# Kernel optimization log

Hardware: AMD Instinct MI355X
Metric: run time of the kernel (lower is better)

Reference implementation:

```python
import jax, jax.numpy as jnp
import numpy as np

N, NQ, NV, NE = 4, 256, 512, 256


def setup_inputs() -> dict:
    key = jax.random.key(0)
    ks = jax.random.split(key, 6)
    scale = 1.0 / np.sqrt(NE)
    return {
        "query": jax.random.normal(ks[0], (N, NQ, NE), dtype=jnp.float32),
        "context": jax.random.normal(ks[1], (N, NV, NE), dtype=jnp.float32),
        "memory": jax.random.normal(ks[2], (N, NV, NE), dtype=jnp.float32),
        "w_logit": jax.random.normal(ks[3], (NE,), dtype=jnp.float32) * scale,
        "b_logit": jnp.zeros((), dtype=jnp.float32),
        "temp": jnp.ones((), dtype=jnp.float32),
        "w_reduce": jax.random.normal(ks[4], (NE, NE), dtype=jnp.float32) * scale,
        "b_reduce": jnp.zeros((NE,), dtype=jnp.float32),
    }


def reference(query, context, memory, w_logit, b_logit, temp, w_reduce, b_reduce):
    # Additive (Bahdanau) attention, single-head branch of the torch module.
    # qc: [N, nQ, nV, nE] -- the large broadcast-add + tanh intermediate
    qc = jnp.tanh(query[:, :, None, :] + context[:, None, :, :])
    # fc_logit: Linear(nE -> 1), squeeze last dim -> [N, nQ, nV]
    logits = jnp.einsum("nqve,e->nqv", qc, w_logit) + b_logit
    probs = jax.nn.softmax(logits / temp, axis=2)
    # bmm(probs, memory) -> [N, nQ, nE], then leaky_relu (torch default slope 0.01)
    heads = jax.nn.leaky_relu(jnp.einsum("nqv,nve->nqe", probs, memory), negative_slope=0.01)
    # fc_reduceheads: Linear(nE -> nE), torch semantics y = x @ W.T + b
    return heads @ w_reduce.T + b_reduce
```

## Files before the change

### kernel.cpp

```cpp
#include <hip/hip_runtime.h>
#include <math.h>

#define N_B   4
#define NQ_   256
#define NV_   512
#define NE_   256

#define QSCALE 2.8853900817779268f

__device__ __forceinline__ float wave_reduce_sum(float v) {
#pragma unroll
    for (int m = 32; m > 0; m >>= 1) v += __shfl_xor(v, m, 64);
    return v;
}

__global__ __launch_bounds__(256) void prep_kernel(const float* __restrict__ C,
                                                   const float* __restrict__ W,
                                                   float* __restrict__ EC,
                                                   float* __restrict__ WT) {
    __shared__ float tile[64][65];
    const int b = blockIdx.x;
    const int col = threadIdx.x & 63, row4 = threadIdx.x >> 6;
    if (b < 128) {
        const int n  = b >> 5;
        const int e0 = ((b >> 3) & 3) * 64;
        const int v0 = (b & 7) * 64;
        const float* src = C + ((size_t)n * NV_ + v0) * NE_ + e0;
#pragma unroll
        for (int r = 0; r < 16; ++r) {
            const int vl = row4 + r * 4;
            tile[vl][col] = __builtin_amdgcn_exp2f(src[(size_t)vl * NE_ + col] * QSCALE);
        }
        __syncthreads();
        float* dst = EC + ((size_t)n * NE_ + e0) * NV_ + v0;
#pragma unroll
        for (int r = 0; r < 16; ++r) {
            const int el = row4 + r * 4;
            dst[(size_t)el * NV_ + col] = tile[col][el];
        }
    } else {
        const int bb = b - 128;
        const int r0 = (bb >> 2) * 64, c0 = (bb & 3) * 64;
        const float* src = W + (size_t)r0 * NE_ + c0;
#pragma unroll
        for (int r = 0; r < 16; ++r) {
            const int rl = row4 + r * 4;
            tile[rl][col] = src[(size_t)rl * NE_ + col];
        }
        __syncthreads();
        float* dst = WT + (size_t)c0 * NE_ + r0;
#pragma unroll
        for (int r = 0; r < 16; ++r) {
            const int cl = row4 + r * 4;
            dst[(size_t)cl * NE_ + col] = tile[col][cl];
        }
    }
}

#define QTA 4
__global__ __launch_bounds__(256, 8) void logits_kernel(
    const float* __restrict__ Q,
    const float* __restrict__ EC,
    const float* __restrict__ WL,
    float* __restrict__ S)
{
    const int n  = blockIdx.z;
    const int q0 = blockIdx.y * QTA;
    const int v0 = blockIdx.x * 64;
    const int tid = threadIdx.x;
    const int wv = tid >> 6, ln = tid & 63;

    __shared__ __align__(16) float s_q[NE_][QTA];
    __shared__ float s_w[NE_];
    __shared__ float s_part[4][QTA][64];

    {
        const int e = tid;
        s_w[e] = WL[e];
#pragma unroll
        for (int j = 0; j < QTA; ++j)
            s_q[e][j] = __builtin_amdgcn_exp2f(
                Q[((size_t)n * NQ_ + q0 + j) * NE_ + e] * QSCALE);
    }
    __syncthreads();

    const float* ec = EC + (size_t)n * NE_ * NV_ + v0 + ln;
    float acc0 = 0.f, acc1 = 0.f, acc2 = 0.f, acc3 = 0.f;
    const int e0 = wv * 64;
#pragma unroll 4
    for (int e = e0; e < e0 + 64; e += 2) {
        const float c0 = ec[(size_t)e * NV_];
        const float c1 = ec[(size_t)(e + 1) * NV_];
        const float4 qa = *(const float4*)s_q[e];
        const float4 qb = *(const float4*)s_q[e + 1];
        const float w0 = s_w[e], w1 = s_w[e + 1];
        {
            const float a = fmaf(c0, qa.x, 1.0f);
            const float b = fmaf(c1, qb.x, 1.0f);
            const float num = fmaf(w1, a, w0 * b);
            acc0 = fmaf(num, __builtin_amdgcn_rcpf(a * b), acc0);
        }
        {
            const float a = fmaf(c0, qa.y, 1.0f);
            const float b = fmaf(c1, qb.y, 1.0f);
            const float num = fmaf(w1, a, w0 * b);
            acc1 = fmaf(num, __builtin_amdgcn_rcpf(a * b), acc1);
        }
        {
            const float a = fmaf(c0, qa.z, 1.0f);
            const float b = fmaf(c1, qb.z, 1.0f);
            const float num = fmaf(w1, a, w0 * b);
            acc2 = fmaf(num, __builtin_amdgcn_rcpf(a * b), acc2);
        }
        {
            const float a = fmaf(c0, qa.w, 1.0f);
            const float b = fmaf(c1, qb.w, 1.0f);
            const float num = fmaf(w1, a, w0 * b);
            acc3 = fmaf(num, __builtin_amdgcn_rcpf(a * b), acc3);
        }
    }
    s_part[wv][0][ln] = acc0;
    s_part[wv][1][ln] = acc1;
    s_part[wv][2][ln] = acc2;
    s_part[wv][3][ln] = acc3;
    __syncthreads();

    {
        const int j = tid >> 6, l = tid & 63;
        const float s = s_part[0][j][l] + s_part[1][j][l]
                      + s_part[2][j][l] + s_part[3][j][l];
        S[((size_t)n * NQ_ + q0 + j) * NV_ + v0 + l] = s;
    }
}

#define QTB 4
#define NWB 8
__global__ __launch_bounds__(512) void attn_out(
    const float* __restrict__ S,
    const float* __restrict__ M,
    const float* __restrict__ TEMP,
    const float* __restrict__ WRT,
    const float* __restrict__ BR,
    float* __restrict__ OUT)
{
    const int n  = blockIdx.y;
    const int q0 = blockIdx.x * QTB;
    const int tid = threadIdx.x;
    const int wv = tid >> 6, ln = tid & 63;

    __shared__ __align__(16) float s_prob[QTB][NV_];
    __shared__ __align__(16) float s_part[NWB][QTB][NE_];
    __shared__ __align__(16) float s_heads[QTB][NE_];

    if (wv < QTB) {
        const float scale = -2.0f / TEMP[0];
        const float* srow = S + ((size_t)n * NQ_ + q0 + wv) * NV_;
        float l[NV_ / 64];
        float mx = -1e30f;
#pragma unroll
        for (int k = 0; k < NV_ / 64; ++k) {
            l[k] = srow[ln + 64 * k] * scale;
            mx = fmaxf(mx, l[k]);
        }
#pragma unroll
        for (int m = 32; m > 0; m >>= 1) mx = fmaxf(mx, __shfl_xor(mx, m, 64));
        float sum = 0.0f;
#pragma unroll
        for (int k = 0; k < NV_ / 64; ++k) {
            l[k] = __expf(l[k] - mx);
            sum += l[k];
        }
        sum = wave_reduce_sum(sum);
        const float inv = 1.0f / sum;
#pragma unroll
        for (int k = 0; k < NV_ / 64; ++k) s_prob[wv][ln + 64 * k] = l[k] * inv;
    }
    __syncthreads();

    {
        const float4* M4 = (const float4*)(M + (size_t)n * NV_ * NE_);
        float4 h[QTB];
#pragma unroll
        for (int t = 0; t < QTB; ++t) h[t] = make_float4(0.f, 0.f, 0.f, 0.f);
        const int v0 = wv * (NV_ / NWB);
#pragma unroll 2
        for (int v = v0; v < v0 + NV_ / NWB; ++v) {
            const float4 m = M4[v * (NE_ / 4) + ln];
#pragma unroll
            for (int t = 0; t < QTB; ++t) {
                const float p = s_prob[t][v];
                h[t].x = fmaf(p, m.x, h[t].x);
                h[t].y = fmaf(p, m.y, h[t].y);
                h[t].z = fmaf(p, m.z, h[t].z);
                h[t].w = fmaf(p, m.w, h[t].w);
            }
        }
#pragma unroll
        for (int t = 0; t < QTB; ++t) ((float4*)s_part[wv][t])[ln] = h[t];
    }
    __syncthreads();

#pragma unroll
    for (int i = tid; i < QTB * NE_; i += 512) {
        const int t = i >> 8, e = i & (NE_ - 1);
        float s = 0.0f;
#pragma unroll
        for (int w = 0; w < NWB; ++w) s += s_part[w][t][e];
        s_heads[t][e] = (s > 0.0f) ? s : 0.01f * s;
    }
    __syncthreads();

    {
        const int t0 = (tid >> 8) * 2;
        const int ep = tid & 255;
        const float* w = WRT + ep;
        float a0 = 0.f, a1 = 0.f;
#pragma unroll 8
        for (int e = 0; e < NE_; ++e) {
            const float wv_ = w[(size_t)e * NE_];
            a0 = fmaf(s_heads[t0][e], wv_, a0);
            a1 = fmaf(s_heads[t0 + 1][e], wv_, a1);
        }
        const float b = BR[ep];
        OUT[((size_t)n * NQ_ + q0 + t0) * NE_ + ep]     = a0 + b;
        OUT[((size_t)n * NQ_ + q0 + t0 + 1) * NE_ + ep] = a1 + b;
    }
}

extern "C" void kernel_launch(void* const* d_in, const int* in_sizes, int n_in,
                              void* d_out, int out_size, void* d_ws, size_t ws_size,
                              hipStream_t stream) {
    const float* Q  = (const float*)d_in[0];
    const float* C  = (const float*)d_in[1];
    const float* M  = (const float*)d_in[2];
    const float* WL = (const float*)d_in[3];
    const float* T  = (const float*)d_in[5];
    const float* WR = (const float*)d_in[6];
    const float* BR = (const float*)d_in[7];
    float* OUT = (float*)d_out;

    float* EC  = (float*)d_ws;
    float* WRT = EC + (size_t)N_B * NE_ * NV_;
    float* S   = WRT + (size_t)NE_ * NE_;

    prep_kernel<<<dim3(144), 256, 0, stream>>>(C, WR, EC, WRT);

    dim3 ga(NV_ / 64, NQ_ / QTA, N_B);
    logits_kernel<<<ga, 256, 0, stream>>>(Q, EC, WL, S);

    dim3 gb(NQ_ / QTB, N_B);
    attn_out<<<gb, 512, 0, stream>>>(S, M, T, WRT, BR, OUT);
}
```

Measured before the change: 109.1 us.

## Fuse logits, softmax and output projection into one 1024-thread kernel

Merges the logits kernel and the attention-output kernel into one kernel per 4-query tile with 1024 threads. Each thread computes full logits for one v over half of e, and softmax runs directly from registers, which removes the global logits buffer and one launch. EC is repacked as interleaved e-pairs so each thread does a float2 load. In exchange the grid shrinks to 256 blocks of 1024 threads with about 70KB of shared memory, which may lower occupancy and latency hiding in the logits loop.

```diff
diff --git a/kernel.cpp b/kernel.cpp
--- a/kernel.cpp
+++ b/kernel.cpp
@@ -7,6 +7,7 @@
 #define NE_   256
 
 #define QSCALE 2.8853900817779268f
+#define QTF 4
 
 __device__ __forceinline__ float wave_reduce_sum(float v) {
 #pragma unroll
@@ -32,11 +33,12 @@
             tile[vl][col] = __builtin_amdgcn_exp2f(src[(size_t)vl * NE_ + col] * QSCALE);
         }
         __syncthreads();
-        float* dst = EC + ((size_t)n * NE_ + e0) * NV_ + v0;
-#pragma unroll
-        for (int r = 0; r < 16; ++r) {
-            const int el = row4 + r * 4;
-            dst[(size_t)el * NV_ + col] = tile[col][el];
+        float2* dst = (float2*)EC + ((size_t)n * (NE_ / 2) + (e0 >> 1)) * NV_ + v0;
+#pragma unroll
+        for (int rr = 0; rr < 8; ++rr) {
+            const int pe = rr * 4 + row4;
+            dst[(size_t)pe * NV_ + col] =
+                make_float2(tile[col][2 * pe], tile[col][2 * pe + 1]);
         }
     } else {
         const int bb = b - 128;
@@ -57,173 +59,182 @@
     }
 }
 
-#define QTA 4
-__global__ __launch_bounds__(256, 8) void logits_kernel(
+#define FMA4(h, p, m)                  \
+    h.x = fmaf(p, m.x, h.x);           \
+    h.y = fmaf(p, m.y, h.y);           \
+    h.z = fmaf(p, m.z, h.z);           \
+    h.w = fmaf(p, m.w, h.w)
+
+__global__ __launch_bounds__(1024) void fused_attn(
     const float* __restrict__ Q,
     const float* __restrict__ EC,
     const float* __restrict__ WL,
-    float* __restrict__ S)
-{
-    const int n  = blockIdx.z;
-    const int q0 = blockIdx.y * QTA;
-    const int v0 = blockIdx.x * 64;
-    const int tid = threadIdx.x;
-    const int wv = tid >> 6, ln = tid & 63;
-
-    __shared__ __align__(16) float s_q[NE_][QTA];
-    __shared__ float s_w[NE_];
-    __shared__ float s_part[4][QTA][64];
-
-    {
-        const int e = tid;
-        s_w[e] = WL[e];
-#pragma unroll
-        for (int j = 0; j < QTA; ++j)
-            s_q[e][j] = __builtin_amdgcn_exp2f(
-                Q[((size_t)n * NQ_ + q0 + j) * NE_ + e] * QSCALE);
-    }
-    __syncthreads();
-
-    const float* ec = EC + (size_t)n * NE_ * NV_ + v0 + ln;
-    float acc0 = 0.f, acc1 = 0.f, acc2 = 0.f, acc3 = 0.f;
-    const int e0 = wv * 64;
-#pragma unroll 4
-    for (int e = e0; e < e0 + 64; e += 2) {
-        const float c0 = ec[(size_t)e * NV_];
-        const float c1 = ec[(size_t)(e + 1) * NV_];
-        const float4 qa = *(const float4*)s_q[e];
-        const float4 qb = *(const float4*)s_q[e + 1];
-        const float w0 = s_w[e], w1 = s_w[e + 1];
-        {
-            const float a = fmaf(c0, qa.x, 1.0f);
-            const float b = fmaf(c1, qb.x, 1.0f);
-            const float num = fmaf(w1, a, w0 * b);
-            acc0 = fmaf(num, __builtin_amdgcn_rcpf(a * b), acc0);
-        }
-        {
-            const float a = fmaf(c0, qa.y, 1.0f);
-            const float b = fmaf(c1, qb.y, 1.0f);
-            const float num = fmaf(w1, a, w0 * b);
-            acc1 = fmaf(num, __builtin_amdgcn_rcpf(a * b), acc1);
-        }
-        {
-            const float a = fmaf(c0, qa.z, 1.0f);
-            const float b = fmaf(c1, qb.z, 1.0f);
-            const float num = fmaf(w1, a, w0 * b);
-            acc2 = fmaf(num, __builtin_amdgcn_rcpf(a * b), acc2);
-        }
-        {
-            const float a = fmaf(c0, qa.w, 1.0f);
-            const float b = fmaf(c1, qb.w, 1.0f);
-            const float num = fmaf(w1, a, w0 * b);
-            acc3 = fmaf(num, __builtin_amdgcn_rcpf(a * b), acc3);
-        }
-    }
-    s_part[wv][0][ln] = acc0;
-    s_part[wv][1][ln] = acc1;
-    s_part[wv][2][ln] = acc2;
-    s_part[wv][3][ln] = acc3;
-    __syncthreads();
-
-    {
-        const int j = tid >> 6, l = tid & 63;
-        const float s = s_part[0][j][l] + s_part[1][j][l]
-                      + s_part[2][j][l] + s_part[3][j][l];
-        S[((size_t)n * NQ_ + q0 + j) * NV_ + v0 + l] = s;
-    }
-}
-
-#define QTB 4
-#define NWB 8
-__global__ __launch_bounds__(512) void attn_out(
-    const float* __restrict__ S,
     const float* __restrict__ M,
     const float* __restrict__ TEMP,
     const float* __restrict__ WRT,
     const float* __restrict__ BR,
     float* __restrict__ OUT)
 {
-    const int n  = blockIdx.y;
-    const int q0 = blockIdx.x * QTB;
+    const int n   = blockIdx.y;
+    const int q0  = blockIdx.x * QTF;
     const int tid = threadIdx.x;
-    const int wv = tid >> 6, ln = tid & 63;
-
-    __shared__ __align__(16) float s_prob[QTB][NV_];
-    __shared__ __align__(16) float s_part[NWB][QTB][NE_];
-    __shared__ __align__(16) float s_heads[QTB][NE_];
-
-    if (wv < QTB) {
+    const int wv  = tid >> 6, ln = tid & 63;
+
+    __shared__ __align__(16) float s_q[NE_][QTF];
+    __shared__ __align__(16) float s_w[NE_];
+    __shared__ __align__(16) float s_prob[QTF][NV_];
+    __shared__ __align__(16) float s_sp[QTF][NV_];
+    __shared__ __align__(16) float s_part[16][QTF][NE_];
+    __shared__ __align__(16) float s_heads[QTF][NE_];
+    __shared__ __align__(16) float s_gp[QTF][NE_];
+    __shared__ float s_sum[QTF][8];
+
+    {
+        const int e = tid & 255;
+        const int g = tid >> 8;
+        s_q[e][g] = __builtin_amdgcn_exp2f(
+            Q[((size_t)n * NQ_ + q0 + g) * NE_ + e] * QSCALE);
+        if (g == 0) s_w[e] = WL[e];
+    }
+    __syncthreads();
+
+    const int v  = tid & 511;
+    const int eh = tid >> 9;
+    float acc0 = 0.f, acc1 = 0.f, acc2 = 0.f, acc3 = 0.f;
+    {
+        const float2* ec2 =
+            (const float2*)EC + ((size_t)n * (NE_ / 2) + eh * 64) * NV_ + v;
+#pragma unroll 4
+        for (int pe = 0; pe < 64; ++pe) {
+            const float2 c = ec2[(size_t)pe * NV_];
+            const int e = eh * 128 + 2 * pe;
+            const float4 qa = *(const float4*)s_q[e];
+            const float4 qb = *(const float4*)s_q[e + 1];
+            const float2 w  = *(const float2*)&s_w[e];
+            {
+                const float a = fmaf(c.x, qa.x, 1.0f);
+                const float b = fmaf(c.y, qb.x, 1.0f);
+                const float num = fmaf(w.y, a, w.x * b);
+                acc0 = fmaf(num, __builtin_amdgcn_rcpf(a * b), acc0);
+            }
+            {
+                const float a = fmaf(c.x, qa.y, 1.0f);
+                const float b = fmaf(c.y, qb.y, 1.0f);
+                const float num = fmaf(w.y, a, w.x * b);
+                acc1 = fmaf(num, __builtin_amdgcn_rcpf(a * b), acc1);
+            }
+            {
+                const float a = fmaf(c.x, qa.z, 1.0f);
+                const float b = fmaf(c.y, qb.z, 1.0f);
+                const float num = fmaf(w.y, a, w.x * b);
+                acc2 = fmaf(num, __builtin_amdgcn_rcpf(a * b), acc2);
+            }
+            {
+                const float a = fmaf(c.x, qa.w, 1.0f);
+                const float b = fmaf(c.y, qb.w, 1.0f);
+                const float num = fmaf(w.y, a, w.x * b);
+                acc3 = fmaf(num, __builtin_amdgcn_rcpf(a * b), acc3);
+            }
+        }
+    }
+    if (eh) {
+        s_sp[0][v] = acc0; s_sp[1][v] = acc1;
+        s_sp[2][v] = acc2; s_sp[3][v] = acc3;
+    }
+    __syncthreads();
+
+    float p0 = 0.f, p1 = 0.f, p2 = 0.f, p3 = 0.f;
+    if (!eh) {
         const float scale = -2.0f / TEMP[0];
-        const float* srow = S + ((size_t)n * NQ_ + q0 + wv) * NV_;
-        float l[NV_ / 64];
-        float mx = -1e30f;
-#pragma unroll
-        for (int k = 0; k < NV_ / 64; ++k) {
-            l[k] = srow[ln + 64 * k] * scale;
-            mx = fmaxf(mx, l[k]);
-        }
-#pragma unroll
-        for (int m = 32; m > 0; m >>= 1) mx = fmaxf(mx, __shfl_xor(mx, m, 64));
-        float sum = 0.0f;
-#pragma unroll
-        for (int k = 0; k < NV_ / 64; ++k) {
-            l[k] = __expf(l[k] - mx);
-            sum += l[k];
-        }
-        sum = wave_reduce_sum(sum);
-        const float inv = 1.0f / sum;
-#pragma unroll
-        for (int k = 0; k < NV_ / 64; ++k) s_prob[wv][ln + 64 * k] = l[k] * inv;
+        p0 = __expf((acc0 + s_sp[0][v]) * scale);
+        p1 = __expf((acc1 + s_sp[1][v]) * scale);
+        p2 = __expf((acc2 + s_sp[2][v]) * scale);
+        p3 = __expf((acc3 + s_sp[3][v]) * scale);
+        const float r0 = wave_reduce_sum(p0);
+        const float r1 = wave_reduce_sum(p1);
+        const float r2 = wave_reduce_sum(p2);
+        const float r3 = wave_reduce_sum(p3);
+        if (ln == 0) {
+            s_sum[0][wv] = r0; s_sum[1][wv] = r1;
+            s_sum[2][wv] = r2; s_sum[3][wv] = r3;
+        }
+    }
+    __syncthreads();
+    if (!eh) {
+        float t0 = 0.f, t1 = 0.f, t2 = 0.f, t3 = 0.f;
+#pragma unroll
+        for (int w = 0; w < 8; ++w) {
+            t0 += s_sum[0][w]; t1 += s_sum[1][w];
+            t2 += s_sum[2][w]; t3 += s_sum[3][w];
+        }
+        s_prob[0][v] = p0 * (1.0f / t0);
+        s_prob[1][v] = p1 * (1.0f / t1);
+        s_prob[2][v] = p2 * (1.0f / t2);
+        s_prob[3][v] = p3 * (1.0f / t3);
     }
     __syncthreads();
 
     {
         const float4* M4 = (const float4*)(M + (size_t)n * NV_ * NE_);
-        float4 h[QTB];
-#pragma unroll
-        for (int t = 0; t < QTB; ++t) h[t] = make_float4(0.f, 0.f, 0.f, 0.f);
-        const int v0 = wv * (NV_ / NWB);
+        float4 h0 = make_float4(0.f, 0.f, 0.f, 0.f);
+        float4 h1 = h0, h2 = h0, h3 = h0;
+        const int v0w = wv * 32;
 #pragma unroll 2
-        for (int v = v0; v < v0 + NV_ / NWB; ++v) {
-            const float4 m = M4[v * (NE_ / 4) + ln];
-#pragma unroll
-            for (int t = 0; t < QTB; ++t) {
-                const float p = s_prob[t][v];
-                h[t].x = fmaf(p, m.x, h[t].x);
-                h[t].y = fmaf(p, m.y, h[t].y);
-                h[t].z = fmaf(p, m.z, h[t].z);
-                h[t].w = fmaf(p, m.w, h[t].w);
-            }
-        }
-#pragma unroll
-        for (int t = 0; t < QTB; ++t) ((float4*)s_part[wv][t])[ln] = h[t];
-    }
-    __syncthreads();
-
-#pragma unroll
-    for (int i = tid; i < QTB * NE_; i += 512) {
-        const int t = i >> 8, e = i & (NE_ - 1);
-        float s = 0.0f;
-#pragma unroll
-        for (int w = 0; w < NWB; ++w) s += s_part[w][t][e];
+        for (int vb = v0w; vb < v0w + 32; vb += 4) {
+            const float4 pq0 = *(const float4*)&s_prob[0][vb];
+            const float4 pq1 = *(const float4*)&s_prob[1][vb];
+            const float4 pq2 = *(const float4*)&s_prob[2][vb];
+            const float4 pq3 = *(const float4*)&s_prob[3][vb];
+            float4 mm;
+            mm = M4[(size_t)(vb + 0) * (NE_ / 4) + ln];
+            FMA4(h0, pq0.x, mm); FMA4(h1, pq1.x, mm);
+            FMA4(h2, pq2.x, mm); FMA4(h3, pq3.x, mm);
+            mm = M4[(size_t)(vb + 1) * (NE_ / 4) + ln];
+            FMA4(h0, pq0.y, mm); FMA4(h1, pq1.y, mm);
+            FMA4(h2, pq2.y, mm); FMA4(h3, pq3.y, mm);
+            mm = M4[(size_t)(vb + 2) * (NE_ / 4) + ln];
+            FMA4(h0, pq0.z, mm); FMA4(h1, pq1.z, mm);
+            FMA4(h2, pq2.z, mm); FMA4(h3, pq3.z, mm);
+            mm = M4[(size_t)(vb + 3) * (NE_ / 4) + ln];
+            FMA4(h0, pq0.w, mm); FMA4(h1, pq1.w, mm);
+            FMA4(h2, pq2.w, mm); FMA4(h3, pq3.w, mm);
+        }
+        ((float4*)s_part[wv][0])[ln] = h0;
+        ((float4*)s_part[wv][1])[ln] = h1;
+        ((float4*)s_part[wv][2])[ln] = h2;
+        ((float4*)s_part[wv][3])[ln] = h3;
+    }
+    __syncthreads();
+
+    {
+        const int t = tid >> 8, e = tid & 255;
+        float s = 0.f;
+#pragma unroll
+        for (int w = 0; w < 16; ++w) s += s_part[w][t][e];
         s_heads[t][e] = (s > 0.0f) ? s : 0.01f * s;
     }
     __syncthreads();
 
     {
-        const int t0 = (tid >> 8) * 2;
-        const int ep = tid & 255;
-        const float* w = WRT + ep;
+        const int eh2 = tid >> 9;
+        const int tg  = ((tid >> 8) & 1) * 2;
+        const int ep  = tid & 255;
+        const float* wc = WRT + ep;
         float a0 = 0.f, a1 = 0.f;
+        const int e0g = eh2 * 128;
 #pragma unroll 8
-        for (int e = 0; e < NE_; ++e) {
-            const float wv_ = w[(size_t)e * NE_];
-            a0 = fmaf(s_heads[t0][e], wv_, a0);
-            a1 = fmaf(s_heads[t0 + 1][e], wv_, a1);
-        }
-        const float b = BR[ep];
-        OUT[((size_t)n * NQ_ + q0 + t0) * NE_ + ep]     = a0 + b;
-        OUT[((size_t)n * NQ_ + q0 + t0 + 1) * NE_ + ep] = a1 + b;
+        for (int e = e0g; e < e0g + 128; ++e) {
+            const float ww = wc[(size_t)e * NE_];
+            a0 = fmaf(s_heads[tg][e], ww, a0);
+            a1 = fmaf(s_heads[tg + 1][e], ww, a1);
+        }
+        if (eh2) { s_gp[tg][ep] = a0; s_gp[tg + 1][ep] = a1; }
+        __syncthreads();
+        if (!eh2) {
+            const float b = BR[ep];
+            OUT[((size_t)n * NQ_ + q0 + tg) * NE_ + ep]     = a0 + s_gp[tg][ep] + b;
+            OUT[((size_t)n * NQ_ + q0 + tg + 1) * NE_ + ep] = a1 + s_gp[tg + 1][ep] + b;
+        }
     }
 }
 
@@ -241,13 +252,9 @@
 
     float* EC  = (float*)d_ws;
     float* WRT = EC + (size_t)N_B * NE_ * NV_;
-    float* S   = WRT + (size_t)NE_ * NE_;
 
     prep_kernel<<<dim3(144), 256, 0, stream>>>(C, WR, EC, WRT);
 
-    dim3 ga(NV_ / 64, NQ_ / QTA, N_B);
-    logits_kernel<<<ga, 256, 0, stream>>>(Q, EC, WL, S);
-
-    dim3 gb(NQ_ / QTB, N_B);
-    attn_out<<<gb, 512, 0, stream>>>(S, M, T, WRT, BR, OUT);
-}
+    dim3 gf(NQ_ / QTF, N_B);
+    fused_attn<<<gf, 1024, 0, stream>>>(Q, EC, WL, M, T, WRT, BR, OUT);
+}
```

After: 99.62 us. 1.09x faster.
